# Performance work log

Measured on AMD Instinct MI355X. Metric: run time of the kernel, lower is better.

Reference implementation:

```python
import jax, jax.numpy as jnp
import numpy as np
import math

B, S, D, H = 4, 2048, 1024, 16
HD = D // H  # head_dim = 64


def setup_inputs() -> dict:
    key = jax.random.key(0)
    ks = jax.random.split(key, 7)
    s = 0.02
    return {
        "q": jax.random.normal(ks[0], (B, S, D), jnp.float32),
        "k": jax.random.normal(ks[1], (B, S, D), jnp.float32),
        "v": jax.random.normal(ks[2], (B, S, D), jnp.float32),
        "wq": jax.random.normal(ks[3], (D, D), jnp.float32) * s,
        "wk": jax.random.normal(ks[4], (D, D), jnp.float32) * s,
        "wv": jax.random.normal(ks[5], (D, D), jnp.float32) * s,
        "wo": jax.random.normal(ks[6], (D, D), jnp.float32) * s,
    }


def reference(q, k, v, wq, wk, wv, wo):
    # Linear (no bias): y = x @ W.T, W is (out, in)
    xq = jnp.einsum('bsd,ed->bse', q, wq).reshape(B, S, H, HD).transpose(0, 2, 1, 3)
    xk = jnp.einsum('bsd,ed->bse', k, wk).reshape(B, S, H, HD).transpose(0, 2, 1, 3)
    xv = jnp.einsum('bsd,ed->bse', v, wv).reshape(B, S, H, HD).transpose(0, 2, 1, 3)
    scores = jnp.einsum('bhqd,bhkd->bhqk', xq, xk) / math.sqrt(HD)  # [B,H,S,S]
    causal = jnp.tril(jnp.ones((S, S), dtype=bool))
    scores = jnp.where(causal[None, None], scores, jnp.float32(-jnp.inf))
    probs = jax.nn.softmax(scores, axis=-1)  # dropout p=0 -> identity
    out = jnp.einsum('bhqk,bhkd->bhqd', probs, xv)  # [B,H,S,HD]
    out = out.transpose(0, 2, 1, 3).reshape(B, S, D)
    return jnp.einsum('bsd,ed->bse', out, wo)
```

## Files before the change

kernel.cpp:

```cpp
#include <hip/hip_runtime.h>

#define SS 2048
#define DD 1024
#define HH 16
#define HD 64
#define MM 8192

typedef unsigned short ushort_t;
typedef __attribute__((ext_vector_type(8))) short short8;
typedef __attribute__((ext_vector_type(4))) float f32x4;
typedef __attribute__((ext_vector_type(4))) unsigned short us4;

__device__ __forceinline__ ushort_t f2bf(float f) {
    union { float f; unsigned u; } x; x.f = f;
    unsigned r = x.u + 0x7fffu + ((x.u >> 16) & 1u);
    return (ushort_t)(r >> 16);
}
__device__ __forceinline__ float bf2f(ushort_t h) {
    union { unsigned u; float f; } x; x.u = ((unsigned)h) << 16; return x.f;
}
__device__ __forceinline__ unsigned pack_bf2(float a, float b) {
    union { float f; unsigned u; } x, y; x.f = a; y.f = b;
    return __builtin_amdgcn_perm(y.u, x.u, 0x07060302u);
}

__device__ __forceinline__ void async16(const void* g, void* l) {
    __builtin_amdgcn_global_load_lds(
        (const __attribute__((address_space(1))) unsigned int*)g,
        (__attribute__((address_space(3))) unsigned int*)l, 16, 0, 0);
}

__global__ void cvt_w(const float* __restrict__ wq, const float* __restrict__ wk,
                      const float* __restrict__ wv, const float* __restrict__ wo,
                      ushort_t* __restrict__ dst) {
    int i = (blockIdx.x * 256 + threadIdx.x) * 4;
    int w = i >> 20, j = i & 1048575;
    const float* src = (w == 0) ? wq : (w == 1) ? wk : (w == 2) ? wv : wo;
    float4 f = *(const float4*)(src + j);
    us4 o; o.x = f2bf(f.x); o.y = f2bf(f.y); o.z = f2bf(f.z); o.w = f2bf(f.w);
    *(us4*)(dst + i) = o;
}

__device__ __forceinline__ void epi_scatter(f32x4 acc[4][4], int m0, int n0,
                                            int mode, void* Yv) {
    int tid = threadIdx.x;
    int w = tid >> 6, lane = tid & 63;
    int l16 = lane & 15, quad = lane >> 4;
    int wm = (w >> 1) * 64, wn = (w & 1) * 64;
    #pragma unroll
    for (int mt = 0; mt < 4; ++mt) {
        #pragma unroll
        for (int r = 0; r < 4; ++r) {
            int row = m0 + wm + mt * 16 + quad * 4 + r;
            #pragma unroll
            for (int nt = 0; nt < 4; ++nt) {
                int col = n0 + wn + nt * 16 + l16;
                float vf = acc[mt][nt][r];
                if (mode == 2) {
                    ((float*)Yv)[(size_t)row * DD + col] = vf;
                } else {
                    ushort_t vh = f2bf(vf);
                    int b = row >> 11, s = row & 2047;
                    int h = col >> 6,  hd = col & 63;
                    if (mode == 0) {
                        ((ushort_t*)Yv)[(((size_t)b * HH + h) * SS + s) * HD + hd] = vh;
                    } else {
                        int sp = (s & ~63) | (((s & 15) << 2) | ((s >> 4) & 3));
                        ((ushort_t*)Yv)[(((size_t)b * HH + h) * HD + hd) * SS + sp] = vh;
                    }
                }
            }
        }
    }
}

__global__ __launch_bounds__(256) void proj3f(const float* __restrict__ q,
                                              const float* __restrict__ k,
                                              const float* __restrict__ v,
                                              const ushort_t* __restrict__ Wall,
                                              ushort_t* __restrict__ xq,
                                              ushort_t* __restrict__ xk,
                                              ushort_t* __restrict__ xvT) {
    __shared__ __align__(16) ushort_t As[128 * 32];
    __shared__ __align__(16) ushort_t Bs[128 * 32];
    int tid = threadIdx.x;
    int w = tid >> 6, lane = tid & 63;
    int l16 = lane & 15, quad = lane >> 4;
    int mat   = (int)(blockIdx.x >> 9);
    int inner = (int)(blockIdx.x & 511);
    int m0 = (inner & 63) * 128;
    int n0 = (inner >> 6) * 128;
    const float*    A  = (mat == 0) ? q : (mat == 1) ? k : v;
    const ushort_t* Bw = Wall + ((size_t)mat << 20);
    int wm = (w >> 1) * 64, wn = (w & 1) * 64;

    f32x4 acc[4][4];
    #pragma unroll
    for (int i = 0; i < 4; ++i)
        #pragma unroll
        for (int j = 0; j < 4; ++j) acc[i][j] = (f32x4){0.f, 0.f, 0.f, 0.f};

    int g0 = w * 64 + lane, r0 = g0 >> 2, j0 = ((g0 & 3) ^ (r0 & 3)) * 8;
    int g1 = g0 + 256,      r1 = g1 >> 2, j1 = ((g1 & 3) ^ (r1 & 3)) * 8;
    ushort_t* bD0 = Bs + (size_t)(w * 64) * 8;
    ushort_t* bD1 = Bs + (size_t)(256 + w * 64) * 8;
    int ar0 = tid >> 2,         ac0 = tid & 3;
    int ar1 = (tid + 256) >> 2, ac1 = (tid + 256) & 3;
    ushort_t* aW0 = As + ar0 * 32 + ((ac0 ^ (ar0 & 3)) * 8);
    ushort_t* aW1 = As + ar1 * 32 + ((ac1 ^ (ar1 & 3)) * 8);
    int swA = (quad ^ (l16 & 3)) * 8;

    for (int k0 = 0; k0 < DD; k0 += 32) {
        __syncthreads();
        async16(Bw + (size_t)(n0 + r0) * DD + k0 + j0, bD0);
        async16(Bw + (size_t)(n0 + r1) * DD + k0 + j1, bD1);
        {
            const float* s0 = A + (size_t)(m0 + ar0) * DD + k0 + ac0 * 8;
            const float* s1 = A + (size_t)(m0 + ar1) * DD + k0 + ac1 * 8;
            float4 f0 = *(const float4*)s0, f1 = *(const float4*)(s0 + 4);
            float4 f2 = *(const float4*)s1, f3 = *(const float4*)(s1 + 4);
            uint4 p0 = { pack_bf2(f0.x, f0.y), pack_bf2(f0.z, f0.w),
                         pack_bf2(f1.x, f1.y), pack_bf2(f1.z, f1.w) };
            uint4 p1 = { pack_bf2(f2.x, f2.y), pack_bf2(f2.z, f2.w),
                         pack_bf2(f3.x, f3.y), pack_bf2(f3.z, f3.w) };
            *(uint4*)aW0 = p0;
            *(uint4*)aW1 = p1;
        }
        __syncthreads();

        short8 af[4], bfr[4];
        #pragma unroll
        for (int t = 0; t < 4; ++t) {
            af[t]  = *(const short8*)&As[(wm + t * 16 + l16) * 32 + swA];
            bfr[t] = *(const short8*)&Bs[(wn + t * 16 + l16) * 32 + swA];
        }
        #pragma unroll
        for (int mt = 0; mt < 4; ++mt)
            #pragma unroll
            for (int nt = 0; nt < 4; ++nt)
                acc[mt][nt] = __builtin_amdgcn_mfma_f32_16x16x32_bf16(af[mt], bfr[nt], acc[mt][nt], 0, 0, 0);
    }

    void* Y = (mat == 0) ? (void*)xq : (mat == 1) ? (void*)xk : (void*)xvT;
    epi_scatter(acc, m0, n0, (mat == 2) ? 1 : 0, Y);
}

__global__ __launch_bounds__(256) void out_gemm(const ushort_t* __restrict__ Abf,
                                                const ushort_t* __restrict__ Bw,
                                                float* __restrict__ Y) {
    __shared__ __align__(16) ushort_t As[128 * 32];
    __shared__ __align__(16) ushort_t Bs[128 * 32];
    int tid = threadIdx.x;
    int w = tid >> 6, lane = tid & 63;
    int l16 = lane & 15, quad = lane >> 4;
    int m0 = (int)(blockIdx.x & 63) * 128;
    int n0 = (int)(blockIdx.x >> 6) * 128;
    int wm = (w >> 1) * 64, wn = (w & 1) * 64;

    f32x4 acc[4][4];
    #pragma unroll
    for (int i = 0; i < 4; ++i)
        #pragma unroll
        for (int j = 0; j < 4; ++j) acc[i][j] = (f32x4){0.f, 0.f, 0.f, 0.f};

    int g0 = w * 64 + lane, r0 = g0 >> 2, j0 = ((g0 & 3) ^ (r0 & 3)) * 8;
    int g1 = g0 + 256,      r1 = g1 >> 2, j1 = ((g1 & 3) ^ (r1 & 3)) * 8;
    ushort_t* aD0 = As + (size_t)(w * 64) * 8;
    ushort_t* aD1 = As + (size_t)(256 + w * 64) * 8;
    ushort_t* bD0 = Bs + (size_t)(w * 64) * 8;
    ushort_t* bD1 = Bs + (size_t)(256 + w * 64) * 8;
    int swA = (quad ^ (l16 & 3)) * 8;

    for (int k0 = 0; k0 < DD; k0 += 32) {
        __syncthreads();
        async16(Abf + (size_t)(m0 + r0) * DD + k0 + j0, aD0);
        async16(Abf + (size_t)(m0 + r1) * DD + k0 + j1, aD1);
        async16(Bw  + (size_t)(n0 + r0) * DD + k0 + j0, bD0);
        async16(Bw  + (size_t)(n0 + r1) * DD + k0 + j1, bD1);
        __syncthreads();

        short8 af[4], bfr[4];
        #pragma unroll
        for (int t = 0; t < 4; ++t) {
            af[t]  = *(const short8*)&As[(wm + t * 16 + l16) * 32 + swA];
            bfr[t] = *(const short8*)&Bs[(wn + t * 16 + l16) * 32 + swA];
        }
        #pragma unroll
        for (int mt = 0; mt < 4; ++mt)
            #pragma unroll
            for (int nt = 0; nt < 4; ++nt)
                acc[mt][nt] = __builtin_amdgcn_mfma_f32_16x16x32_bf16(af[mt], bfr[nt], acc[mt][nt], 0, 0, 0);
    }
    epi_scatter(acc, m0, n0, 2, Y);
}

__global__ __launch_bounds__(256) void attn_kernel(const ushort_t* __restrict__ xq,
                                                   const ushort_t* __restrict__ xk,
                                                   const ushort_t* __restrict__ xvT,
                                                   ushort_t* __restrict__ ao) {
    __shared__ __align__(16) ushort_t Ksm[64 * 64];
    __shared__ __align__(16) ushort_t Vsm[64 * 64];
    __shared__ __align__(16) ushort_t Psm[4][16 * 72];

    int tid = threadIdx.x;
    int w = tid >> 6, lane = tid & 63;
    int l16 = lane & 15, quad = lane >> 4;
    int bh = blockIdx.x & 63;
    int p  = blockIdx.x >> 6;
    int b = bh >> 4, h = bh & 15;

    const ushort_t* Q  = xq  + (size_t)bh * SS * HD;
    const ushort_t* K  = xk  + (size_t)bh * SS * HD;
    const ushort_t* VT = xvT + (size_t)bh * HD * SS;

    int g0 = w * 64 + lane, r0 = g0 >> 3, j0 = ((g0 & 7) ^ (r0 & 7)) * 8;
    int g1 = g0 + 256,      r1 = g1 >> 3, j1 = ((g1 & 7) ^ (r1 & 7)) * 8;
    ushort_t* kD0 = Ksm + (size_t)(w * 64) * 8;
    ushort_t* kD1 = Ksm + (size_t)(256 + w * 64) * 8;
    ushort_t* vD0 = Vsm + (size_t)(w * 64) * 8;
    ushort_t* vD1 = Vsm + (size_t)(256 + w * 64) * 8;

    short8 ones;
    #pragma unroll
    for (int i = 0; i < 8; ++i) ones[i] = (short)0x3F80;

    const float CS = 0.125f * 1.44269504f;

    for (int ph = 0; ph < 2; ++ph) {
        int qt = ph ? (31 - p) : p;
        int qb = qt * 64;
        int qmin = qb + w * 16;

        short8 aq[2];
        #pragma unroll
        for (int kc = 0; kc < 2; ++kc) {
            short8 t = *(const short8*)(Q + (size_t)(qmin + l16) * HD + kc * 32 + quad * 8);
            #pragma unroll
            for (int i = 0; i < 8; ++i)
                t[i] = (short)f2bf(bf2f((ushort_t)t[i]) * CS);
            aq[kc] = t;
        }

        f32x4 o[4];
        #pragma unroll
        for (int dt = 0; dt < 4; ++dt) o[dt] = (f32x4){0.f, 0.f, 0.f, 0.f};
        f32x4 lacc = (f32x4){0.f, 0.f, 0.f, 0.f};

        for (int kt = 0; kt <= qt; ++kt) {
            int kb = kt * 64;
            __syncthreads();
            async16(K  + (size_t)(kb + r0) * HD + j0, kD0);
            async16(K  + (size_t)(kb + r1) * HD + j1, kD1);
            async16(VT + (size_t)r0 * SS + kb + j0, vD0);
            async16(VT + (size_t)r1 * SS + kb + j1, vD1);
            __syncthreads();

            f32x4 sc[4];
            #pragma unroll
            for (int nt = 0; nt < 4; ++nt) {
                int row = nt * 16 + l16;
                short8 bk0 = *(const short8*)&Ksm[row * 64 + ((0 + quad) ^ (l16 & 7)) * 8];
                short8 bk1 = *(const short8*)&Ksm[row * 64 + ((4 + quad) ^ (l16 & 7)) * 8];
                f32x4 c = (f32x4){0.f, 0.f, 0.f, 0.f};
                c = __builtin_amdgcn_mfma_f32_16x16x32_bf16(aq[0], bk0, c, 0, 0, 0);
                c = __builtin_amdgcn_mfma_f32_16x16x32_bf16(aq[1], bk1, c, 0, 0, 0);
                sc[nt] = c;
            }

            bool msk = (kt == qt);
            #pragma unroll
            for (int r = 0; r < 4; ++r) {
                float e0, e1, e2, e3;
                if (msk) {
                    int qg = qmin + quad * 4 + r;
                    e0 = (kb +  0 + l16 <= qg) ? __builtin_amdgcn_exp2f(sc[0][r]) : 0.f;
                    e1 = (kb + 16 + l16 <= qg) ? __builtin_amdgcn_exp2f(sc[1][r]) : 0.f;
                    e2 = (kb + 32 + l16 <= qg) ? __builtin_amdgcn_exp2f(sc[2][r]) : 0.f;
                    e3 = (kb + 48 + l16 <= qg) ? __builtin_amdgcn_exp2f(sc[3][r]) : 0.f;
                } else {
                    e0 = __builtin_amdgcn_exp2f(sc[0][r]);
                    e1 = __builtin_amdgcn_exp2f(sc[1][r]);
                    e2 = __builtin_amdgcn_exp2f(sc[2][r]);
                    e3 = __builtin_amdgcn_exp2f(sc[3][r]);
                }
                uint2 pk = { pack_bf2(e0, e1), pack_bf2(e2, e3) };
                *(uint2*)&Psm[w][(quad * 4 + r) * 72 + l16 * 4] = pk;
            }

            asm volatile("s_waitcnt lgkmcnt(0)" ::: "memory");

            #pragma unroll
            for (int kc = 0; kc < 2; ++kc) {
                short8 ap = *(const short8*)&Psm[w][l16 * 72 + kc * 32 + quad * 8];
                lacc = __builtin_amdgcn_mfma_f32_16x16x32_bf16(ap, ones, lacc, 0, 0, 0);
                #pragma unroll
                for (int dt = 0; dt < 4; ++dt) {
                    int row = dt * 16 + l16;
                    short8 bv = *(const short8*)&Vsm[row * 64 + ((kc * 4 + quad) ^ (l16 & 7)) * 8];
                    o[dt] = __builtin_amdgcn_mfma_f32_16x16x32_bf16(ap, bv, o[dt], 0, 0, 0);
                }
            }
        }

        #pragma unroll
        for (int r = 0; r < 4; ++r) {
            float inv = 1.0f / lacc[r];
            int qg = qmin + quad * 4 + r;
            #pragma unroll
            for (int dt = 0; dt < 4; ++dt)
                ao[((size_t)(b * SS + qg)) * DD + h * HD + dt * 16 + l16] = f2bf(o[dt][r] * inv);
        }
    }
}

extern "C" void kernel_launch(void* const* d_in, const int* in_sizes, int n_in,
                              void* d_out, int out_size, void* d_ws, size_t ws_size,
                              hipStream_t stream) {
    const float* q  = (const float*)d_in[0];
    const float* k  = (const float*)d_in[1];
    const float* v  = (const float*)d_in[2];
    const float* wq = (const float*)d_in[3];
    const float* wk = (const float*)d_in[4];
    const float* wv = (const float*)d_in[5];
    const float* wo = (const float*)d_in[6];
    float* out = (float*)d_out;

    ushort_t* wbf = (ushort_t*)d_ws;
    ushort_t* xq  = wbf + 4194304ull;
    ushort_t* xk  = xq  + 8388608ull;
    ushort_t* xvT = xk  + 8388608ull;
    ushort_t* ao  = xvT + 8388608ull;

    cvt_w<<<4096, 256, 0, stream>>>(wq, wk, wv, wo, wbf);
    proj3f<<<1536, 256, 0, stream>>>(q, k, v, wbf, xq, xk, xvT);
    attn_kernel<<<1024, 256, 0, stream>>>(xq, xk, xvT, ao);
    out_gemm<<<512, 256, 0, stream>>>(ao, wbf + 3145728ull, out);
}
```

Before: 357.9 us.

## Double-buffer shared-memory tiles in projection, output GEMM and attention kernels

Each of the three kernels now keeps two shared-memory buffers for its K-loop operands. The next tile's global loads (async copies, plus the fp32 A reads in the projection kernel) are issued before the MFMA work on the current tile, and only one barrier is used per iteration instead of two. The goal is to hide global-load latency behind matrix-core work and cut barrier stalls. The cost is double the LDS footprint, which may lower occupancy, and extra live registers for the prefetched A values.

```diff
diff --git a/kernel.cpp b/kernel.cpp
--- a/kernel.cpp
+++ b/kernel.cpp
@@ -81,8 +81,8 @@
                                               ushort_t* __restrict__ xq,
                                               ushort_t* __restrict__ xk,
                                               ushort_t* __restrict__ xvT) {
-    __shared__ __align__(16) ushort_t As[128 * 32];
-    __shared__ __align__(16) ushort_t Bs[128 * 32];
+    __shared__ __align__(16) ushort_t As[2][128 * 32];
+    __shared__ __align__(16) ushort_t Bs[2][128 * 32];
     int tid = threadIdx.x;
     int w = tid >> 6, lane = tid & 63;
     int l16 = lane & 15, quad = lane >> 4;
@@ -102,43 +102,60 @@
 
     int g0 = w * 64 + lane, r0 = g0 >> 2, j0 = ((g0 & 3) ^ (r0 & 3)) * 8;
     int g1 = g0 + 256,      r1 = g1 >> 2, j1 = ((g1 & 3) ^ (r1 & 3)) * 8;
-    ushort_t* bD0 = Bs + (size_t)(w * 64) * 8;
-    ushort_t* bD1 = Bs + (size_t)(256 + w * 64) * 8;
     int ar0 = tid >> 2,         ac0 = tid & 3;
     int ar1 = (tid + 256) >> 2, ac1 = (tid + 256) & 3;
-    ushort_t* aW0 = As + ar0 * 32 + ((ac0 ^ (ar0 & 3)) * 8);
-    ushort_t* aW1 = As + ar1 * 32 + ((ac1 ^ (ar1 & 3)) * 8);
+    int aw0 = ar0 * 32 + ((ac0 ^ (ar0 & 3)) * 8);
+    int aw1 = ar1 * 32 + ((ac1 ^ (ar1 & 3)) * 8);
+    const float* Arow0 = A + (size_t)(m0 + ar0) * DD + ac0 * 8;
+    const float* Arow1 = A + (size_t)(m0 + ar1) * DD + ac1 * 8;
     int swA = (quad ^ (l16 & 3)) * 8;
 
-    for (int k0 = 0; k0 < DD; k0 += 32) {
+    {
+        float4 f0 = *(const float4*)(Arow0), f1 = *(const float4*)(Arow0 + 4);
+        float4 f2 = *(const float4*)(Arow1), f3 = *(const float4*)(Arow1 + 4);
+        async16(Bw + (size_t)(n0 + r0) * DD + j0, &Bs[0][(size_t)(w * 64) * 8]);
+        async16(Bw + (size_t)(n0 + r1) * DD + j1, &Bs[0][(size_t)(256 + w * 64) * 8]);
+        uint4 p0 = { pack_bf2(f0.x, f0.y), pack_bf2(f0.z, f0.w),
+                     pack_bf2(f1.x, f1.y), pack_bf2(f1.z, f1.w) };
+        uint4 p1 = { pack_bf2(f2.x, f2.y), pack_bf2(f2.z, f2.w),
+                     pack_bf2(f3.x, f3.y), pack_bf2(f3.z, f3.w) };
+        *(uint4*)&As[0][aw0] = p0;
+        *(uint4*)&As[0][aw1] = p1;
+    }
+
+    for (int kk = 0; kk < 32; ++kk) {
+        int c = kk & 1;
         __syncthreads();
-        async16(Bw + (size_t)(n0 + r0) * DD + k0 + j0, bD0);
-        async16(Bw + (size_t)(n0 + r1) * DD + k0 + j1, bD1);
-        {
-            const float* s0 = A + (size_t)(m0 + ar0) * DD + k0 + ac0 * 8;
-            const float* s1 = A + (size_t)(m0 + ar1) * DD + k0 + ac1 * 8;
-            float4 f0 = *(const float4*)s0, f1 = *(const float4*)(s0 + 4);
-            float4 f2 = *(const float4*)s1, f3 = *(const float4*)(s1 + 4);
+        bool pf = (kk < 31);
+        float4 f0, f1, f2, f3;
+        if (pf) {
+            int k1 = (kk + 1) * 32;
+            f0 = *(const float4*)(Arow0 + k1); f1 = *(const float4*)(Arow0 + k1 + 4);
+            f2 = *(const float4*)(Arow1 + k1); f3 = *(const float4*)(Arow1 + k1 + 4);
+            async16(Bw + (size_t)(n0 + r0) * DD + k1 + j0, &Bs[c ^ 1][(size_t)(w * 64) * 8]);
+            async16(Bw + (size_t)(n0 + r1) * DD + k1 + j1, &Bs[c ^ 1][(size_t)(256 + w * 64) * 8]);
+        }
+
+        short8 af[4], bfr[4];
+        #pragma unroll
+        for (int t = 0; t < 4; ++t) {
+            af[t]  = *(const short8*)&As[c][(wm + t * 16 + l16) * 32 + swA];
+            bfr[t] = *(const short8*)&Bs[c][(wn + t * 16 + l16) * 32 + swA];
+        }
+        #pragma unroll
+        for (int mt = 0; mt < 4; ++mt)
+            #pragma unroll
+            for (int nt = 0; nt < 4; ++nt)
+                acc[mt][nt] = __builtin_amdgcn_mfma_f32_16x16x32_bf16(af[mt], bfr[nt], acc[mt][nt], 0, 0, 0);
+
+        if (pf) {
             uint4 p0 = { pack_bf2(f0.x, f0.y), pack_bf2(f0.z, f0.w),
                          pack_bf2(f1.x, f1.y), pack_bf2(f1.z, f1.w) };
             uint4 p1 = { pack_bf2(f2.x, f2.y), pack_bf2(f2.z, f2.w),
                          pack_bf2(f3.x, f3.y), pack_bf2(f3.z, f3.w) };
-            *(uint4*)aW0 = p0;
-            *(uint4*)aW1 = p1;
-        }
-        __syncthreads();
-
-        short8 af[4], bfr[4];
-        #pragma unroll
-        for (int t = 0; t < 4; ++t) {
-            af[t]  = *(const short8*)&As[(wm + t * 16 + l16) * 32 + swA];
-            bfr[t] = *(const short8*)&Bs[(wn + t * 16 + l16) * 32 + swA];
-        }
-        #pragma unroll
-        for (int mt = 0; mt < 4; ++mt)
-            #pragma unroll
-            for (int nt = 0; nt < 4; ++nt)
-                acc[mt][nt] = __builtin_amdgcn_mfma_f32_16x16x32_bf16(af[mt], bfr[nt], acc[mt][nt], 0, 0, 0);
+            *(uint4*)&As[c ^ 1][aw0] = p0;
+            *(uint4*)&As[c ^ 1][aw1] = p1;
+        }
     }
 
     void* Y = (mat == 0) ? (void*)xq : (mat == 1) ? (void*)xk : (void*)xvT;
@@ -148,8 +165,8 @@
 __global__ __launch_bounds__(256) void out_gemm(const ushort_t* __restrict__ Abf,
                                                 const ushort_t* __restrict__ Bw,
                                                 float* __restrict__ Y) {
-    __shared__ __align__(16) ushort_t As[128 * 32];
-    __shared__ __align__(16) ushort_t Bs[128 * 32];
+    __shared__ __align__(16) ushort_t As[2][128 * 32];
+    __shared__ __align__(16) ushort_t Bs[2][128 * 32];
     int tid = threadIdx.x;
     int w = tid >> 6, lane = tid & 63;
     int l16 = lane & 15, quad = lane >> 4;
@@ -165,25 +182,28 @@
 
     int g0 = w * 64 + lane, r0 = g0 >> 2, j0 = ((g0 & 3) ^ (r0 & 3)) * 8;
     int g1 = g0 + 256,      r1 = g1 >> 2, j1 = ((g1 & 3) ^ (r1 & 3)) * 8;
-    ushort_t* aD0 = As + (size_t)(w * 64) * 8;
-    ushort_t* aD1 = As + (size_t)(256 + w * 64) * 8;
-    ushort_t* bD0 = Bs + (size_t)(w * 64) * 8;
-    ushort_t* bD1 = Bs + (size_t)(256 + w * 64) * 8;
     int swA = (quad ^ (l16 & 3)) * 8;
 
-    for (int k0 = 0; k0 < DD; k0 += 32) {
+    async16(Abf + (size_t)(m0 + r0) * DD + j0, &As[0][(size_t)(w * 64) * 8]);
+    async16(Abf + (size_t)(m0 + r1) * DD + j1, &As[0][(size_t)(256 + w * 64) * 8]);
+    async16(Bw  + (size_t)(n0 + r0) * DD + j0, &Bs[0][(size_t)(w * 64) * 8]);
+    async16(Bw  + (size_t)(n0 + r1) * DD + j1, &Bs[0][(size_t)(256 + w * 64) * 8]);
+
+    for (int kk = 0; kk < 32; ++kk) {
+        int c = kk & 1;
         __syncthreads();
-        async16(Abf + (size_t)(m0 + r0) * DD + k0 + j0, aD0);
-        async16(Abf + (size_t)(m0 + r1) * DD + k0 + j1, aD1);
-        async16(Bw  + (size_t)(n0 + r0) * DD + k0 + j0, bD0);
-        async16(Bw  + (size_t)(n0 + r1) * DD + k0 + j1, bD1);
-        __syncthreads();
-
+        if (kk < 31) {
+            int k1 = (kk + 1) * 32;
+            async16(Abf + (size_t)(m0 + r0) * DD + k1 + j0, &As[c ^ 1][(size_t)(w * 64) * 8]);
+            async16(Abf + (size_t)(m0 + r1) * DD + k1 + j1, &As[c ^ 1][(size_t)(256 + w * 64) * 8]);
+            async16(Bw  + (size_t)(n0 + r0) * DD + k1 + j0, &Bs[c ^ 1][(size_t)(w * 64) * 8]);
+            async16(Bw  + (size_t)(n0 + r1) * DD + k1 + j1, &Bs[c ^ 1][(size_t)(256 + w * 64) * 8]);
+        }
         short8 af[4], bfr[4];
         #pragma unroll
         for (int t = 0; t < 4; ++t) {
-            af[t]  = *(const short8*)&As[(wm + t * 16 + l16) * 32 + swA];
-            bfr[t] = *(const short8*)&Bs[(wn + t * 16 + l16) * 32 + swA];
+            af[t]  = *(const short8*)&As[c][(wm + t * 16 + l16) * 32 + swA];
+            bfr[t] = *(const short8*)&Bs[c][(wn + t * 16 + l16) * 32 + swA];
         }
         #pragma unroll
         for (int mt = 0; mt < 4; ++mt)
@@ -198,8 +218,8 @@
                                                    const ushort_t* __restrict__ xk,
                                                    const ushort_t* __restrict__ xvT,
                                                    ushort_t* __restrict__ ao) {
-    __shared__ __align__(16) ushort_t Ksm[64 * 64];
-    __shared__ __align__(16) ushort_t Vsm[64 * 64];
+    __shared__ __align__(16) ushort_t Ksm[2][64 * 64];
+    __shared__ __align__(16) ushort_t Vsm[2][64 * 64];
     __shared__ __align__(16) ushort_t Psm[4][16 * 72];
 
     int tid = threadIdx.x;
@@ -215,10 +235,6 @@
 
     int g0 = w * 64 + lane, r0 = g0 >> 3, j0 = ((g0 & 7) ^ (r0 & 7)) * 8;
     int g1 = g0 + 256,      r1 = g1 >> 3, j1 = ((g1 & 7) ^ (r1 & 7)) * 8;
-    ushort_t* kD0 = Ksm + (size_t)(w * 64) * 8;
-    ushort_t* kD1 = Ksm + (size_t)(256 + w * 64) * 8;
-    ushort_t* vD0 = Vsm + (size_t)(w * 64) * 8;
-    ushort_t* vD1 = Vsm + (size_t)(256 + w * 64) * 8;
 
     short8 ones;
     #pragma unroll
@@ -246,25 +262,34 @@
         for (int dt = 0; dt < 4; ++dt) o[dt] = (f32x4){0.f, 0.f, 0.f, 0.f};
         f32x4 lacc = (f32x4){0.f, 0.f, 0.f, 0.f};
 
+        __syncthreads();
+        async16(K  + (size_t)r0 * HD + j0, &Ksm[0][(size_t)(w * 64) * 8]);
+        async16(K  + (size_t)r1 * HD + j1, &Ksm[0][(size_t)(256 + w * 64) * 8]);
+        async16(VT + (size_t)r0 * SS + j0, &Vsm[0][(size_t)(w * 64) * 8]);
+        async16(VT + (size_t)r1 * SS + j1, &Vsm[0][(size_t)(256 + w * 64) * 8]);
+
         for (int kt = 0; kt <= qt; ++kt) {
             int kb = kt * 64;
+            int c = kt & 1;
             __syncthreads();
-            async16(K  + (size_t)(kb + r0) * HD + j0, kD0);
-            async16(K  + (size_t)(kb + r1) * HD + j1, kD1);
-            async16(VT + (size_t)r0 * SS + kb + j0, vD0);
-            async16(VT + (size_t)r1 * SS + kb + j1, vD1);
-            __syncthreads();
+            if (kt < qt) {
+                int kb1 = kb + 64;
+                async16(K  + (size_t)(kb1 + r0) * HD + j0, &Ksm[c ^ 1][(size_t)(w * 64) * 8]);
+                async16(K  + (size_t)(kb1 + r1) * HD + j1, &Ksm[c ^ 1][(size_t)(256 + w * 64) * 8]);
+                async16(VT + (size_t)r0 * SS + kb1 + j0, &Vsm[c ^ 1][(size_t)(w * 64) * 8]);
+                async16(VT + (size_t)r1 * SS + kb1 + j1, &Vsm[c ^ 1][(size_t)(256 + w * 64) * 8]);
+            }
 
             f32x4 sc[4];
             #pragma unroll
             for (int nt = 0; nt < 4; ++nt) {
                 int row = nt * 16 + l16;
-                short8 bk0 = *(const short8*)&Ksm[row * 64 + ((0 + quad) ^ (l16 & 7)) * 8];
-                short8 bk1 = *(const short8*)&Ksm[row * 64 + ((4 + quad) ^ (l16 & 7)) * 8];
-                f32x4 c = (f32x4){0.f, 0.f, 0.f, 0.f};
-                c = __builtin_amdgcn_mfma_f32_16x16x32_bf16(aq[0], bk0, c, 0, 0, 0);
-                c = __builtin_amdgcn_mfma_f32_16x16x32_bf16(aq[1], bk1, c, 0, 0, 0);
-                sc[nt] = c;
+                short8 bk0 = *(const short8*)&Ksm[c][row * 64 + ((0 + quad) ^ (l16 & 7)) * 8];
+                short8 bk1 = *(const short8*)&Ksm[c][row * 64 + ((4 + quad) ^ (l16 & 7)) * 8];
+                f32x4 cc = (f32x4){0.f, 0.f, 0.f, 0.f};
+                cc = __builtin_amdgcn_mfma_f32_16x16x32_bf16(aq[0], bk0, cc, 0, 0, 0);
+                cc = __builtin_amdgcn_mfma_f32_16x16x32_bf16(aq[1], bk1, cc, 0, 0, 0);
+                sc[nt] = cc;
             }
 
             bool msk = (kt == qt);
@@ -296,7 +321,7 @@
                 #pragma unroll
                 for (int dt = 0; dt < 4; ++dt) {
                     int row = dt * 16 + l16;
-                    short8 bv = *(const short8*)&Vsm[row * 64 + ((kc * 4 + quad) ^ (l16 & 7)) * 8];
+                    short8 bv = *(const short8*)&Vsm[c][row * 64 + ((kc * 4 + quad) ^ (l16 & 7)) * 8];
                     o[dt] = __builtin_amdgcn_mfma_f32_16x16x32_bf16(ap, bv, o[dt], 0, 0, 0);
                 }
             }
```

Measured after the change: 346.6 us. 1.03x faster.
